# Kernel optimization log

Hardware: AMD Instinct MI355X
Metric: run time of the kernel (lower is better)

## Reference

```python
import jax, jax.numpy as jnp
import numpy as np

NUM_KNOTS = 64
HEAD_DIM = 4
SCALE = 0.5  # 1/sqrt(4)


def setup_inputs() -> dict:
    key = jax.random.key(0)
    ks = jax.random.split(key, 6)
    B, L, D = 4, 128, 256
    s = 1.0 / np.sqrt(D)
    return {
        "x": jax.random.normal(ks[0], (B, L, D), dtype=jnp.float32),
        "Wq": jax.random.normal(ks[1], (D, D), dtype=jnp.float32) * s,
        "Wk": jax.random.normal(ks[2], (D, D), dtype=jnp.float32) * s,
        "Wv": jax.random.normal(ks[3], (D, D), dtype=jnp.float32) * s,
        "Wo": jax.random.normal(ks[4], (D, D), dtype=jnp.float32) * s,
        "bo": jnp.zeros((D,), dtype=jnp.float32),
    }


def reference(x, Wq, Wk, Wv, Wo, bo):
    # x: [B, L, D], D = NUM_KNOTS * HEAD_DIM = 256
    B, L, D = x.shape
    N = L * NUM_KNOTS  # flattened 'knot' sequence length
    # nn.Linear applies x @ W.T
    q = (x @ Wq.T).reshape(B, N, HEAD_DIM)
    k = (x @ Wk.T).reshape(B, N, HEAD_DIM)
    v = (x @ Wv.T).reshape(B, N, HEAD_DIM)
    # full attention over the length-N knot sequence (head_dim = 4)
    logits = jnp.einsum("bnd,bmd->bnm", q, k) * SCALE  # [B, N, N]
    attn = jax.nn.softmax(logits, axis=-1)
    out = jnp.einsum("bnm,bmd->bnd", attn, v).reshape(B, L, D)
    return out @ Wo.T + bo
```

## Files before the change

### kernel.cpp

```cpp
#include <hip/hip_runtime.h>

#define NQ 8192
#define BLROWS 512
#define DIM 256
#define KSLICES 16

#define QSCALE 0.7213475204444817f

typedef float v2f __attribute__((ext_vector_type(2)));
typedef float v4f __attribute__((ext_vector_type(4)));

__device__ __forceinline__ float ex2(float x) {
#if __has_builtin(__builtin_amdgcn_exp2f)
    return __builtin_amdgcn_exp2f(x);
#else
    return exp2f(x);
#endif
}

__global__ __launch_bounds__(256) void qkv_proj(
    const float* __restrict__ x,
    const float* __restrict__ Wq, const float* __restrict__ Wk,
    const float* __restrict__ Wv,
    float* __restrict__ Qb, float* __restrict__ Kb, float* __restrict__ Vb)
{
    const int m = blockIdx.y;
    const float* W = (m == 0) ? Wq : (m == 1) ? Wk : Wv;
    float* C       = (m == 0) ? Qb : (m == 1) ? Kb : Vb;
    const float sc = (m == 0) ? QSCALE : 1.0f;
    const int j  = threadIdx.x;
    const int rb = blockIdx.x * 4;

    float acc[4] = {0.f, 0.f, 0.f, 0.f};
    const float4* __restrict__ W4 = reinterpret_cast<const float4*>(W + j * DIM);
    const float*  __restrict__ A0 = x + rb * DIM;

    #pragma unroll 4
    for (int d4 = 0; d4 < DIM / 4; ++d4) {
        const float4 w = W4[d4];
        #pragma unroll
        for (int r = 0; r < 4; ++r) {
            const float4 a = reinterpret_cast<const float4*>(A0 + r * DIM)[d4];
            acc[r] = fmaf(a.x, w.x, acc[r]);
            acc[r] = fmaf(a.y, w.y, acc[r]);
            acc[r] = fmaf(a.z, w.z, acc[r]);
            acc[r] = fmaf(a.w, w.w, acc[r]);
        }
    }
    #pragma unroll
    for (int r = 0; r < 4; ++r)
        C[(rb + r) * DIM + j] = acc[r] * sc;
}

__global__ __launch_bounds__(256, 4) void attn_partial(
    const float* __restrict__ Q, const float* __restrict__ K,
    const float* __restrict__ V, float* __restrict__ P)
{
    __shared__ __align__(16) float Ksoa[4][512];
    __shared__ __align__(16) float Vsoa[4][512];
    __shared__ float red2[4][256];

    const int t    = threadIdx.x;
    const int lane = t & 63;
    const int w    = __builtin_amdgcn_readfirstlane(t >> 6);
    const int qt   = blockIdx.x;
    const int ks   = blockIdx.y;
    const int b    = blockIdx.z;

    {
        const float4* __restrict__ Kg = reinterpret_cast<const float4*>(K) + b * NQ + ks * 512;
        const float4* __restrict__ Vg = reinterpret_cast<const float4*>(V) + b * NQ + ks * 512;
        const float4 k0 = Kg[t], k1 = Kg[t + 256];
        const float4 v0 = Vg[t], v1 = Vg[t + 256];
        Ksoa[0][t] = k0.x; Ksoa[1][t] = k0.y; Ksoa[2][t] = k0.z; Ksoa[3][t] = k0.w;
        Ksoa[0][t + 256] = k1.x; Ksoa[1][t + 256] = k1.y; Ksoa[2][t + 256] = k1.z; Ksoa[3][t + 256] = k1.w;
        Vsoa[0][t] = v0.x; Vsoa[1][t] = v0.y; Vsoa[2][t] = v0.z; Vsoa[3][t] = v0.w;
        Vsoa[0][t + 256] = v1.x; Vsoa[1][t + 256] = v1.y; Vsoa[2][t + 256] = v1.z; Vsoa[3][t + 256] = v1.w;
    }

    const float4* __restrict__ Qp = reinterpret_cast<const float4*>(Q) + b * NQ + qt * 256;
    v2f qx2[4], qy2[4], qz2[4], qw2[4];
    #pragma unroll
    for (int r = 0; r < 4; ++r) {
        const float4 q = Qp[r * 64 + lane];
        qx2[r] = v2f{q.x, q.x};
        qy2[r] = v2f{q.y, q.y};
        qz2[r] = v2f{q.z, q.z};
        qw2[r] = v2f{q.w, q.w};
    }
    v2f ls2[4], a02[4], a12[4], a22[4], a32[4];
    #pragma unroll
    for (int r = 0; r < 4; ++r) {
        ls2[r] = v2f{0.f, 0.f};
        a02[r] = v2f{0.f, 0.f}; a12[r] = v2f{0.f, 0.f};
        a22[r] = v2f{0.f, 0.f}; a32[r] = v2f{0.f, 0.f};
    }
    __syncthreads();

    const int kbase = w * 128;

    #pragma unroll 2
    for (int jj = 0; jj < 32; ++jj) {
        const int j = kbase + jj * 4;
        const v4f kx4 = *reinterpret_cast<const v4f*>(&Ksoa[0][j]);
        const v4f ky4 = *reinterpret_cast<const v4f*>(&Ksoa[1][j]);
        const v4f kz4 = *reinterpret_cast<const v4f*>(&Ksoa[2][j]);
        const v4f kw4 = *reinterpret_cast<const v4f*>(&Ksoa[3][j]);
        const v4f vx4 = *reinterpret_cast<const v4f*>(&Vsoa[0][j]);
        const v4f vy4 = *reinterpret_cast<const v4f*>(&Vsoa[1][j]);
        const v4f vz4 = *reinterpret_cast<const v4f*>(&Vsoa[2][j]);
        const v4f vw4 = *reinterpret_cast<const v4f*>(&Vsoa[3][j]);
        const v2f kxlo = __builtin_shufflevector(kx4, kx4, 0, 1), kxhi = __builtin_shufflevector(kx4, kx4, 2, 3);
        const v2f kylo = __builtin_shufflevector(ky4, ky4, 0, 1), kyhi = __builtin_shufflevector(ky4, ky4, 2, 3);
        const v2f kzlo = __builtin_shufflevector(kz4, kz4, 0, 1), kzhi = __builtin_shufflevector(kz4, kz4, 2, 3);
        const v2f kwlo = __builtin_shufflevector(kw4, kw4, 0, 1), kwhi = __builtin_shufflevector(kw4, kw4, 2, 3);
        const v2f vxlo = __builtin_shufflevector(vx4, vx4, 0, 1), vxhi = __builtin_shufflevector(vx4, vx4, 2, 3);
        const v2f vylo = __builtin_shufflevector(vy4, vy4, 0, 1), vyhi = __builtin_shufflevector(vy4, vy4, 2, 3);
        const v2f vzlo = __builtin_shufflevector(vz4, vz4, 0, 1), vzhi = __builtin_shufflevector(vz4, vz4, 2, 3);
        const v2f vwlo = __builtin_shufflevector(vw4, vw4, 0, 1), vwhi = __builtin_shufflevector(vw4, vw4, 2, 3);

        #pragma unroll
        for (int r = 0; r < 4; ++r) {
            v2f slo = kxlo * qx2[r];
            slo = __builtin_elementwise_fma(kylo, qy2[r], slo);
            slo = __builtin_elementwise_fma(kzlo, qz2[r], slo);
            slo = __builtin_elementwise_fma(kwlo, qw2[r], slo);
            v2f shi = kxhi * qx2[r];
            shi = __builtin_elementwise_fma(kyhi, qy2[r], shi);
            shi = __builtin_elementwise_fma(kzhi, qz2[r], shi);
            shi = __builtin_elementwise_fma(kwhi, qw2[r], shi);
            const v2f e01 = v2f{ex2(slo[0]), ex2(slo[1])};
            const v2f e23 = v2f{ex2(shi[0]), ex2(shi[1])};
            ls2[r] += e01;
            ls2[r] += e23;
            a02[r] = __builtin_elementwise_fma(e01, vxlo, a02[r]);
            a02[r] = __builtin_elementwise_fma(e23, vxhi, a02[r]);
            a12[r] = __builtin_elementwise_fma(e01, vylo, a12[r]);
            a12[r] = __builtin_elementwise_fma(e23, vyhi, a12[r]);
            a22[r] = __builtin_elementwise_fma(e01, vzlo, a22[r]);
            a22[r] = __builtin_elementwise_fma(e23, vzhi, a22[r]);
            a32[r] = __builtin_elementwise_fma(e01, vwlo, a32[r]);
            a32[r] = __builtin_elementwise_fma(e23, vwhi, a32[r]);
        }
    }

    float* __restrict__ Pb = P + (size_t)((b * KSLICES + ks) * 5) * NQ + qt * 256;
    __syncthreads();

#define RED_ROUND(ARR, cidx)                                              \
    {                                                                     \
        _Pragma("unroll")                                                 \
        for (int r = 0; r < 4; ++r)                                       \
            red2[w][r * 64 + lane] = ARR[r][0] + ARR[r][1];               \
        __syncthreads();                                                  \
        Pb[(cidx) * NQ + t] =                                             \
            red2[0][t] + red2[1][t] + red2[2][t] + red2[3][t];            \
        __syncthreads();                                                  \
    }

    RED_ROUND(ls2, 0)
    RED_ROUND(a02, 1)
    RED_ROUND(a12, 2)
    RED_ROUND(a22, 3)
    RED_ROUND(a32, 4)
#undef RED_ROUND
}

__global__ __launch_bounds__(256) void merge_oproj(
    const float* __restrict__ P, const float* __restrict__ Wo,
    const float* __restrict__ bo, float* __restrict__ out)
{
    __shared__ float aoL[4][DIM];

    const int rb = blockIdx.x * 4;
    const int b  = rb >> 7;
    const int n0 = (rb & 127) * 64;
    const int t  = threadIdx.x;

    {
        float sums[5] = {0.f, 0.f, 0.f, 0.f, 0.f};
        const float* __restrict__ Pb = P + (size_t)(b * KSLICES * 5) * NQ + n0 + t;
        #pragma unroll
        for (int s = 0; s < KSLICES; ++s) {
            #pragma unroll
            for (int c = 0; c < 5; ++c)
                sums[c] += Pb[(s * 5 + c) * NQ];
        }
        const float inv = 1.0f / sums[0];
        const int row = t >> 6;
        const int d0  = (t & 63) * 4;
        aoL[row][d0 + 0] = sums[1] * inv;
        aoL[row][d0 + 1] = sums[2] * inv;
        aoL[row][d0 + 2] = sums[3] * inv;
        aoL[row][d0 + 3] = sums[4] * inv;
    }
    __syncthreads();

    const int j = t;
    float acc[4] = {0.f, 0.f, 0.f, 0.f};
    const float4* __restrict__ W4 = reinterpret_cast<const float4*>(Wo + j * DIM);
    #pragma unroll 4
    for (int d4 = 0; d4 < DIM / 4; ++d4) {
        const float4 wv = W4[d4];
        #pragma unroll
        for (int r = 0; r < 4; ++r) {
            const float4 a = reinterpret_cast<const float4*>(&aoL[r][0])[d4];
            acc[r] = fmaf(a.x, wv.x, acc[r]);
            acc[r] = fmaf(a.y, wv.y, acc[r]);
            acc[r] = fmaf(a.z, wv.z, acc[r]);
            acc[r] = fmaf(a.w, wv.w, acc[r]);
        }
    }
    const float bias = bo[j];
    #pragma unroll
    for (int r = 0; r < 4; ++r)
        out[(rb + r) * DIM + j] = acc[r] + bias;
}

extern "C" void kernel_launch(void* const* d_in, const int* in_sizes, int n_in,
                              void* d_out, int out_size, void* d_ws, size_t ws_size,
                              hipStream_t stream) {
    const float* x  = (const float*)d_in[0];
    const float* Wq = (const float*)d_in[1];
    const float* Wk = (const float*)d_in[2];
    const float* Wv = (const float*)d_in[3];
    const float* Wo = (const float*)d_in[4];
    const float* bo = (const float*)d_in[5];
    float* out = (float*)d_out;

    float* Qb = (float*)d_ws;
    float* Kb = Qb + BLROWS * DIM;
    float* Vb = Kb + BLROWS * DIM;
    float* P  = Vb + BLROWS * DIM;

    qkv_proj<<<dim3(128, 3), 256, 0, stream>>>(x, Wq, Wk, Wv, Qb, Kb, Vb);
    attn_partial<<<dim3(32, KSLICES, 4), 256, 0, stream>>>(Qb, Kb, Vb, P);
    merge_oproj<<<128, 256, 0, stream>>>(P, Wo, bo, out);
}
```

Baseline: 91.59 us.

## Force packed FP32 asm in attention loop and split projections across more blocks

The attention inner loop now uses inline v_pk_mul/v_pk_fma/v_pk_add assembly so the compiler is guaranteed to emit packed FP32 instructions. The QKV projection handles two rows per block instead of four, doubling the grid. The merge/output projection gets a second grid dimension that splits the output columns, with each thread computing two rows. The projection changes are meant to fill more CUs on the small kernels, at the cost of re-reading weights and re-doing the merge in twice as many blocks. Inline asm also limits the compiler's scheduling freedom.

```diff
diff --git a/kernel.cpp b/kernel.cpp
--- a/kernel.cpp
+++ b/kernel.cpp
@@ -16,6 +16,22 @@
 #else
     return exp2f(x);
 #endif
+}
+
+__device__ __forceinline__ v2f pk_mul(v2f a, v2f b) {
+    v2f d;
+    asm("v_pk_mul_f32 %0, %1, %2" : "=v"(d) : "v"(a), "v"(b));
+    return d;
+}
+__device__ __forceinline__ v2f pk_fma(v2f a, v2f b, v2f c) {
+    v2f d;
+    asm("v_pk_fma_f32 %0, %1, %2, %3" : "=v"(d) : "v"(a), "v"(b), "v"(c));
+    return d;
+}
+__device__ __forceinline__ v2f pk_add(v2f a, v2f b) {
+    v2f d;
+    asm("v_pk_add_f32 %0, %1, %2" : "=v"(d) : "v"(a), "v"(b));
+    return d;
 }
 
 __global__ __launch_bounds__(256) void qkv_proj(
@@ -29,17 +45,17 @@
     float* C       = (m == 0) ? Qb : (m == 1) ? Kb : Vb;
     const float sc = (m == 0) ? QSCALE : 1.0f;
     const int j  = threadIdx.x;
-    const int rb = blockIdx.x * 4;
-
-    float acc[4] = {0.f, 0.f, 0.f, 0.f};
+    const int rb = blockIdx.x * 2;
+
+    float acc[2] = {0.f, 0.f};
     const float4* __restrict__ W4 = reinterpret_cast<const float4*>(W + j * DIM);
     const float*  __restrict__ A0 = x + rb * DIM;
 
-    #pragma unroll 4
+    #pragma unroll 8
     for (int d4 = 0; d4 < DIM / 4; ++d4) {
         const float4 w = W4[d4];
         #pragma unroll
-        for (int r = 0; r < 4; ++r) {
+        for (int r = 0; r < 2; ++r) {
             const float4 a = reinterpret_cast<const float4*>(A0 + r * DIM)[d4];
             acc[r] = fmaf(a.x, w.x, acc[r]);
             acc[r] = fmaf(a.y, w.y, acc[r]);
@@ -48,7 +64,7 @@
         }
     }
     #pragma unroll
-    for (int r = 0; r < 4; ++r)
+    for (int r = 0; r < 2; ++r)
         C[(rb + r) * DIM + j] = acc[r] * sc;
 }
 
@@ -121,26 +137,26 @@
 
         #pragma unroll
         for (int r = 0; r < 4; ++r) {
-            v2f slo = kxlo * qx2[r];
-            slo = __builtin_elementwise_fma(kylo, qy2[r], slo);
-            slo = __builtin_elementwise_fma(kzlo, qz2[r], slo);
-            slo = __builtin_elementwise_fma(kwlo, qw2[r], slo);
-            v2f shi = kxhi * qx2[r];
-            shi = __builtin_elementwise_fma(kyhi, qy2[r], shi);
-            shi = __builtin_elementwise_fma(kzhi, qz2[r], shi);
-            shi = __builtin_elementwise_fma(kwhi, qw2[r], shi);
+            v2f slo = pk_mul(kxlo, qx2[r]);
+            slo = pk_fma(kylo, qy2[r], slo);
+            slo = pk_fma(kzlo, qz2[r], slo);
+            slo = pk_fma(kwlo, qw2[r], slo);
+            v2f shi = pk_mul(kxhi, qx2[r]);
+            shi = pk_fma(kyhi, qy2[r], shi);
+            shi = pk_fma(kzhi, qz2[r], shi);
+            shi = pk_fma(kwhi, qw2[r], shi);
             const v2f e01 = v2f{ex2(slo[0]), ex2(slo[1])};
             const v2f e23 = v2f{ex2(shi[0]), ex2(shi[1])};
-            ls2[r] += e01;
-            ls2[r] += e23;
-            a02[r] = __builtin_elementwise_fma(e01, vxlo, a02[r]);
-            a02[r] = __builtin_elementwise_fma(e23, vxhi, a02[r]);
-            a12[r] = __builtin_elementwise_fma(e01, vylo, a12[r]);
-            a12[r] = __builtin_elementwise_fma(e23, vyhi, a12[r]);
-            a22[r] = __builtin_elementwise_fma(e01, vzlo, a22[r]);
-            a22[r] = __builtin_elementwise_fma(e23, vzhi, a22[r]);
-            a32[r] = __builtin_elementwise_fma(e01, vwlo, a32[r]);
-            a32[r] = __builtin_elementwise_fma(e23, vwhi, a32[r]);
+            ls2[r] = pk_add(ls2[r], e01);
+            ls2[r] = pk_add(ls2[r], e23);
+            a02[r] = pk_fma(e01, vxlo, a02[r]);
+            a02[r] = pk_fma(e23, vxhi, a02[r]);
+            a12[r] = pk_fma(e01, vylo, a12[r]);
+            a12[r] = pk_fma(e23, vyhi, a12[r]);
+            a22[r] = pk_fma(e01, vzlo, a22[r]);
+            a22[r] = pk_fma(e23, vzhi, a22[r]);
+            a32[r] = pk_fma(e01, vwlo, a32[r]);
+            a32[r] = pk_fma(e23, vwhi, a32[r]);
         }
     }
 
@@ -196,15 +212,16 @@
     }
     __syncthreads();
 
-    const int j = t;
-    float acc[4] = {0.f, 0.f, 0.f, 0.f};
+    const int j  = blockIdx.y * 128 + (t & 127);
+    const int r0 = (t >> 7) * 2;
+    float acc[2] = {0.f, 0.f};
     const float4* __restrict__ W4 = reinterpret_cast<const float4*>(Wo + j * DIM);
-    #pragma unroll 4
+    #pragma unroll 8
     for (int d4 = 0; d4 < DIM / 4; ++d4) {
         const float4 wv = W4[d4];
         #pragma unroll
-        for (int r = 0; r < 4; ++r) {
-            const float4 a = reinterpret_cast<const float4*>(&aoL[r][0])[d4];
+        for (int r = 0; r < 2; ++r) {
+            const float4 a = reinterpret_cast<const float4*>(&aoL[r0 + r][0])[d4];
             acc[r] = fmaf(a.x, wv.x, acc[r]);
             acc[r] = fmaf(a.y, wv.y, acc[r]);
             acc[r] = fmaf(a.z, wv.z, acc[r]);
@@ -213,8 +230,8 @@
     }
     const float bias = bo[j];
     #pragma unroll
-    for (int r = 0; r < 4; ++r)
-        out[(rb + r) * DIM + j] = acc[r] + bias;
+    for (int r = 0; r < 2; ++r)
+        out[(rb + r0 + r) * DIM + j] = acc[r] + bias;
 }
 
 extern "C" void kernel_launch(void* const* d_in, const int* in_sizes, int n_in,
@@ -233,7 +250,7 @@
     float* Vb = Kb + BLROWS * DIM;
     float* P  = Vb + BLROWS * DIM;
 
-    qkv_proj<<<dim3(128, 3), 256, 0, stream>>>(x, Wq, Wk, Wv, Qb, Kb, Vb);
+    qkv_proj<<<dim3(256, 3), 256, 0, stream>>>(x, Wq, Wk, Wv, Qb, Kb, Vb);
     attn_partial<<<dim3(32, KSLICES, 4), 256, 0, stream>>>(Qb, Kb, Vb, P);
-    merge_oproj<<<128, 256, 0, stream>>>(P, Wo, bo, out);
-}
+    merge_oproj<<<dim3(128, 2), 256, 0, stream>>>(P, Wo, bo, out);
+}
```

Result: slower. 100.7 us (+9.9%).
